# Kernel tuning notes

Measured on AMD Instinct MI355X. Metric: run time of the kernel, lower is better.

Reference implementation:

```python
import jax, jax.numpy as jnp
import numpy as np

B, S, K, N, G = 4, 2048, 4096, 11008, 128


def setup_inputs() -> dict:
    key = jax.random.key(0)
    k1, k2, k3 = jax.random.split(key, 3)
    x = jax.random.normal(k1, (B, S, K), dtype=jnp.float32)
    # packed int4 GPTQ weights: (K/8, N) int32, 8 nibbles per int32
    qweight = jax.random.randint(k2, (K // 8, N), 0, 2147483647, dtype=jnp.int32)
    # per-group scales: (K/G, N), small positive values
    scales = jax.random.uniform(k3, (K // G, N), dtype=jnp.float32) * 0.01 + 0.001
    return {"x": x, "qweight": qweight, "scales": scales, "group_size": G}


def _dequantize(qweight, scales, group_size):
    shifts = jnp.arange(0, 32, 4, dtype=jnp.int32)          # [8]
    w = (qweight[:, None, :] >> shifts[None, :, None]) & 15  # (K/8, 8, N)
    k = w.shape[0] * 8
    w = w.reshape(k, -1)                                     # (K, N) in [0, 15]
    gidx = jnp.arange(k) // group_size                       # (K,)
    # symmetric int4 dequant with per-group, per-output-channel scale
    return (w.astype(scales.dtype) - 8.0) * scales[gidx]     # (K, N)


def reference(x, qweight, scales, group_size):
    Wf = _dequantize(qweight, scales, group_size)            # (K, N)
    return jnp.einsum('bsk,kn->bsn', x, Wf)                  # (B, S, N)
```

## Files before the change

### kernel.cpp

```cpp
#include <hip/hip_runtime.h>
#include <cstdint>
#include <cstddef>

#define M_DIM 8192
#define K_DIM 4096
#define N_DIM 11008
#define NT    (K_DIM / 64)

typedef short bf16x8 __attribute__((ext_vector_type(8)));
typedef float f32x4  __attribute__((ext_vector_type(4)));
typedef unsigned short us8 __attribute__((ext_vector_type(8)));

__device__ __forceinline__ unsigned short f2bf(float f) {
  unsigned int u = __float_as_uint(f);
  u += 0x7FFFu + ((u >> 16) & 1u);
  return (unsigned short)(u >> 16);
}

__global__ __launch_bounds__(256) void cvt_x_kernel(const float* __restrict__ x,
                                                    unsigned short* __restrict__ xb) {
  const int i = blockIdx.x * 256 + threadIdx.x;
  const float4* x4 = (const float4*)x;
  float4 a = x4[(size_t)i * 2];
  float4 b = x4[(size_t)i * 2 + 1];
  us8 o;
  o[0] = f2bf(a.x); o[1] = f2bf(a.y); o[2] = f2bf(a.z); o[3] = f2bf(a.w);
  o[4] = f2bf(b.x); o[5] = f2bf(b.y); o[6] = f2bf(b.z); o[7] = f2bf(b.w);
  *(us8*)(xb + (size_t)i * 8) = o;
}

__global__ __launch_bounds__(256) void dequant_kernel(const int* __restrict__ qw,
                                                      const float* __restrict__ sc,
                                                      unsigned short* __restrict__ wt) {
  const int n0 = blockIdx.x * 64;
  const int k0 = blockIdx.y * 64;
  const int g  = blockIdx.y >> 1;
  __shared__ unsigned short lds[64 * 64];
  const int t = threadIdx.x;
  {
    const int kk_l = t >> 5;
    const int n_l  = (t & 31) * 2;
    const int key  = (n_l >> 1) & 7;
    const int2  q2 = *(const int2*)&qw[(k0 / 8 + kk_l) * N_DIM + n0 + n_l];
    const float2 s2 = *(const float2*)&sc[g * N_DIM + n0 + n_l];
    us8 o0, o1;
#pragma unroll
    for (int j = 0; j < 8; ++j) {
      o0[j] = f2bf((float)(((q2.x >> (4 * j)) & 15) - 8) * s2.x);
      o1[j] = f2bf((float)(((q2.y >> (4 * j)) & 15) - 8) * s2.y);
    }
    const int pch = (kk_l ^ key) * 8;
    *(us8*)&lds[(n_l    ) * 64 + pch] = o0;
    *(us8*)&lds[(n_l + 1) * 64 + pch] = o1;
  }
  __syncthreads();
#pragma unroll
  for (int it = 0; it < 2; ++it) {
    const int idx = t + it * 256;
    const int n_l = idx >> 3;
    const int ch  = idx & 7;
    const int pch = (ch ^ ((n_l >> 1) & 7)) * 8;
    *(us8*)&wt[(size_t)(n0 + n_l) * K_DIM + k0 + ch * 8] = *(const us8*)&lds[n_l * 64 + pch];
  }
}

__global__ __launch_bounds__(512, 2) void gemm_kernel(const unsigned short* __restrict__ A,
                                                      const unsigned short* __restrict__ Bt,
                                                      float* __restrict__ C) {
  __shared__ unsigned short lds[8][8192];
  const int t    = threadIdx.x;
  const int wave = t >> 6;
  const int lane = t & 63;
  const int l15  = lane & 15;
  const int wr   = wave >> 2;
  const int wc   = wave & 3;

  const int bid = blockIdx.x;
  const int wg  = (bid & 7) * 172 + (bid >> 3);
  const int m0  = (wg / 43) * 256;
  const int n0  = (wg % 43) * 256;

  const int sq = (t & 3) ^ ((t >> 3) & 3);
  const unsigned short* gA = A  + (size_t)(m0 + (t >> 2)) * K_DIM + sq * 8;
  const unsigned short* gB = Bt + (size_t)(n0 + (t >> 2)) * K_DIM + sq * 8;

  const int sxo   = ((lane >> 4) ^ ((l15 >> 1) & 3)) << 3;
  const int aoffA = (wr * 128 + l15) * 32 + sxo;
  const int aoffB = (wc * 64  + l15) * 32 + sxo;

  auto stage = [&](const unsigned short* gbase, unsigned short* reg, int h, int tk) {
#pragma unroll
    for (int j = 0; j < 2; ++j) {
      __builtin_amdgcn_global_load_lds(
          (const __attribute__((address_space(1))) unsigned int*)(gbase + (size_t)j * 128 * K_DIM + tk * 64 + h * 32),
          (__attribute__((address_space(3))) unsigned int*)(reg + j * 4096 + t * 8),
          16, 0, 0);
    }
  };

  f32x4 acc[8][4] = {};

  stage(gA, &lds[0][0], 0, 0);
  stage(gB, &lds[4][0], 0, 0);
  stage(gA, &lds[1][0], 1, 0);
  stage(gB, &lds[5][0], 1, 0);
  stage(gA, &lds[2][0], 0, 1);
  stage(gB, &lds[6][0], 0, 1);
  asm volatile("s_waitcnt vmcnt(4)" ::: "memory");
  __builtin_amdgcn_s_barrier();

#pragma unroll 1
  for (int tk = 0; tk < NT; ++tk) {
    const int p = tk & 1;
    const unsigned short* Ah0 = &lds[p * 2 + 0][0];
    const unsigned short* Ah1 = &lds[p * 2 + 1][0];
    const unsigned short* Bh0 = &lds[4 + p * 2 + 0][0];
    const unsigned short* Bh1 = &lds[4 + p * 2 + 1][0];
    unsigned short* stA1 = &lds[(p ^ 1) * 2 + 1][0];
    unsigned short* stB1 = &lds[4 + (p ^ 1) * 2 + 1][0];
    unsigned short* stA2 = &lds[p * 2 + 0][0];
    unsigned short* stB2 = &lds[4 + p * 2 + 0][0];

    bf16x8 a[4], b[4], a2[4];

#pragma unroll
    for (int i = 0; i < 4; ++i) a[i] = *(const bf16x8*)&Ah0[aoffA + i * 512];
#pragma unroll
    for (int i = 0; i < 4; ++i) b[i] = *(const bf16x8*)&Bh0[aoffB + i * 512];
    if (tk + 1 < NT) stage(gA, stA1, 1, tk + 1);
    __builtin_amdgcn_s_barrier();
    __builtin_amdgcn_s_setprio(1);
#pragma unroll
    for (int mi = 0; mi < 4; ++mi)
#pragma unroll
      for (int ni = 0; ni < 4; ++ni)
        acc[mi][ni] = __builtin_amdgcn_mfma_f32_16x16x32_bf16(a[mi], b[ni], acc[mi][ni], 0, 0, 0);
    __builtin_amdgcn_s_setprio(0);
    __builtin_amdgcn_s_barrier();

#pragma unroll
    for (int i = 0; i < 4; ++i) a2[i] = *(const bf16x8*)&Ah0[aoffA + (i + 4) * 512];
    if (tk + 1 < NT) stage(gB, stB1, 1, tk + 1);
    __builtin_amdgcn_s_barrier();
    __builtin_amdgcn_s_setprio(1);
#pragma unroll
    for (int mi = 0; mi < 4; ++mi)
#pragma unroll
      for (int ni = 0; ni < 4; ++ni)
        acc[mi + 4][ni] = __builtin_amdgcn_mfma_f32_16x16x32_bf16(a2[mi], b[ni], acc[mi + 4][ni], 0, 0, 0);
    __builtin_amdgcn_s_setprio(0);
    __builtin_amdgcn_s_barrier();

#pragma unroll
    for (int i = 0; i < 4; ++i) a[i] = *(const bf16x8*)&Ah1[aoffA + i * 512];
#pragma unroll
    for (int i = 0; i < 4; ++i) b[i] = *(const bf16x8*)&Bh1[aoffB + i * 512];
    if (tk + 2 < NT) stage(gA, stA2, 0, tk + 2);
    __builtin_amdgcn_s_barrier();
    __builtin_amdgcn_s_setprio(1);
#pragma unroll
    for (int mi = 0; mi < 4; ++mi)
#pragma unroll
      for (int ni = 0; ni < 4; ++ni)
        acc[mi][ni] = __builtin_amdgcn_mfma_f32_16x16x32_bf16(a[mi], b[ni], acc[mi][ni], 0, 0, 0);
    __builtin_amdgcn_s_setprio(0);
    __builtin_amdgcn_s_barrier();

#pragma unroll
    for (int i = 0; i < 4; ++i) a2[i] = *(const bf16x8*)&Ah1[aoffA + (i + 4) * 512];
    if (tk + 2 < NT) stage(gB, stB2, 0, tk + 2);
    __builtin_amdgcn_s_barrier();
    __builtin_amdgcn_s_setprio(1);
#pragma unroll
    for (int mi = 0; mi < 4; ++mi)
#pragma unroll
      for (int ni = 0; ni < 4; ++ni)
        acc[mi + 4][ni] = __builtin_amdgcn_mfma_f32_16x16x32_bf16(a2[mi], b[ni], acc[mi + 4][ni], 0, 0, 0);
    __builtin_amdgcn_s_setprio(0);
    if (tk + 2 < NT)      { asm volatile("s_waitcnt vmcnt(4)" ::: "memory"); }
    else if (tk + 1 < NT) { asm volatile("s_waitcnt vmcnt(0)" ::: "memory"); }
    __builtin_amdgcn_s_barrier();
  }

  const int cn = n0 + wc * 64 + l15;
  const int rm = m0 + wr * 128 + (lane >> 4) * 4;
#pragma unroll
  for (int mi = 0; mi < 8; ++mi)
#pragma unroll
    for (int ni = 0; ni < 4; ++ni)
#pragma unroll
      for (int r = 0; r < 4; ++r)
        C[(size_t)(rm + mi * 16 + r) * N_DIM + cn + ni * 16] = acc[mi][ni][r];
}

extern "C" void kernel_launch(void* const* d_in, const int* in_sizes, int n_in,
                              void* d_out, int out_size, void* d_ws, size_t ws_size,
                              hipStream_t stream) {
  const float* x  = (const float*)d_in[0];
  const int*   qw = (const int*)d_in[1];
  const float* sc = (const float*)d_in[2];
  float* out = (float*)d_out;

  unsigned short* xb = (unsigned short*)d_ws;
  unsigned short* wt = (unsigned short*)((char*)d_ws + (size_t)M_DIM * K_DIM * 2);

  cvt_x_kernel<<<dim3(M_DIM * K_DIM / (8 * 256)), dim3(256), 0, stream>>>(x, xb);
  dequant_kernel<<<dim3(N_DIM / 64, K_DIM / 64), dim3(256), 0, stream>>>(qw, sc, wt);
  gemm_kernel<<<dim3((N_DIM / 256) * (M_DIM / 256)), dim3(512), 0, stream>>>(xb, wt, out);
}
```

Baseline: 1.143 ms.

## Unroll GEMM K-loop by two with templated stages and finer vmcnt waits

Restructures the GEMM main loop into a two-tile unrolled body with compile-time LDS buffer pointers and constant global offsets, removing per-iteration parity and branch arithmetic. Adds mid-tile vmcnt waits so that half-tile loads are awaited earlier and at finer granularity. It also changes the block-to-tile mapping so that M varies fastest within each group, which shifts L2 reuse patterns. The risk is that the altered wait placement or the new tile order reduces overlap or cache locality.

```diff
diff --git a/kernel.cpp b/kernel.cpp
--- a/kernel.cpp
+++ b/kernel.cpp
@@ -64,123 +64,139 @@
   }
 }
 
+__device__ __forceinline__ void gl_lds(const unsigned short* g, unsigned short* l) {
+  __builtin_amdgcn_global_load_lds(
+      (const __attribute__((address_space(1))) unsigned int*)g,
+      (__attribute__((address_space(3))) unsigned int*)l, 16, 0, 0);
+}
+
+template<int N> __device__ __forceinline__ void vwait() {
+  if constexpr (N == 8) asm volatile("s_waitcnt vmcnt(8)" ::: "memory");
+  if constexpr (N == 4) asm volatile("s_waitcnt vmcnt(4)" ::: "memory");
+  if constexpr (N == 0) asm volatile("s_waitcnt vmcnt(0)" ::: "memory");
+}
+
+__device__ __forceinline__ void mfma16(const bf16x8 (&a)[4], const bf16x8 (&b)[4],
+                                       f32x4 (&acc)[8][4], int mo) {
+#pragma unroll
+  for (int mi = 0; mi < 4; ++mi)
+#pragma unroll
+    for (int ni = 0; ni < 4; ++ni)
+      acc[mi + mo][ni] = __builtin_amdgcn_mfma_f32_16x16x32_bf16(a[mi], b[ni], acc[mi + mo][ni], 0, 0, 0);
+}
+
+template<int W2N, int W1N, bool S12, bool S34>
+__device__ __forceinline__ void tile_step(
+    const unsigned short* Ah0, const unsigned short* Ah1,
+    const unsigned short* Bh0, const unsigned short* Bh1,
+    unsigned short* stA1, unsigned short* stB1,
+    unsigned short* stA2, unsigned short* stB2,
+    const unsigned short* gA0, const unsigned short* gA1,
+    const unsigned short* gB0, const unsigned short* gB1,
+    int off1, int off2, int aoffA, int aoffB, int t8,
+    f32x4 (&acc)[8][4]) {
+  bf16x8 a[4], b[4], a2[4];
+
+#pragma unroll
+  for (int i = 0; i < 4; ++i) a[i] = *(const bf16x8*)&Ah0[aoffA + i * 512];
+#pragma unroll
+  for (int i = 0; i < 4; ++i) b[i] = *(const bf16x8*)&Bh0[aoffB + i * 512];
+  if constexpr (S12) { gl_lds(gA0 + off1, stA1 + t8); gl_lds(gA1 + off1, stA1 + 4096 + t8); }
+  __builtin_amdgcn_s_barrier();
+  __builtin_amdgcn_s_setprio(1);
+  mfma16(a, b, acc, 0);
+  __builtin_amdgcn_s_setprio(0);
+  __builtin_amdgcn_s_barrier();
+
+#pragma unroll
+  for (int i = 0; i < 4; ++i) a2[i] = *(const bf16x8*)&Ah0[aoffA + (i + 4) * 512];
+  if constexpr (S12) { gl_lds(gB0 + off1, stB1 + t8); gl_lds(gB1 + off1, stB1 + 4096 + t8); }
+  __builtin_amdgcn_s_barrier();
+  __builtin_amdgcn_s_setprio(1);
+  mfma16(a2, b, acc, 4);
+  __builtin_amdgcn_s_setprio(0);
+  vwait<W2N>();
+  __builtin_amdgcn_s_barrier();
+
+#pragma unroll
+  for (int i = 0; i < 4; ++i) a[i] = *(const bf16x8*)&Ah1[aoffA + i * 512];
+#pragma unroll
+  for (int i = 0; i < 4; ++i) b[i] = *(const bf16x8*)&Bh1[aoffB + i * 512];
+  if constexpr (S34) { gl_lds(gA0 + off2, stA2 + t8); gl_lds(gA1 + off2, stA2 + 4096 + t8); }
+  __builtin_amdgcn_s_barrier();
+  __builtin_amdgcn_s_setprio(1);
+  mfma16(a, b, acc, 0);
+  __builtin_amdgcn_s_setprio(0);
+  __builtin_amdgcn_s_barrier();
+
+#pragma unroll
+  for (int i = 0; i < 4; ++i) a2[i] = *(const bf16x8*)&Ah1[aoffA + (i + 4) * 512];
+  if constexpr (S34) { gl_lds(gB0 + off2, stB2 + t8); gl_lds(gB1 + off2, stB2 + 4096 + t8); }
+  __builtin_amdgcn_s_barrier();
+  __builtin_amdgcn_s_setprio(1);
+  mfma16(a2, b, acc, 4);
+  __builtin_amdgcn_s_setprio(0);
+  vwait<W1N>();
+  __builtin_amdgcn_s_barrier();
+}
+
 __global__ __launch_bounds__(512, 2) void gemm_kernel(const unsigned short* __restrict__ A,
                                                       const unsigned short* __restrict__ Bt,
                                                       float* __restrict__ C) {
   __shared__ unsigned short lds[8][8192];
+  unsigned short* AE0 = &lds[0][0]; unsigned short* AE1 = &lds[1][0];
+  unsigned short* AO0 = &lds[2][0]; unsigned short* AO1 = &lds[3][0];
+  unsigned short* BE0 = &lds[4][0]; unsigned short* BE1 = &lds[5][0];
+  unsigned short* BO0 = &lds[6][0]; unsigned short* BO1 = &lds[7][0];
+
   const int t    = threadIdx.x;
   const int wave = t >> 6;
   const int lane = t & 63;
   const int l15  = lane & 15;
   const int wr   = wave >> 2;
   const int wc   = wave & 3;
+  const int t8   = t * 8;
 
   const int bid = blockIdx.x;
   const int wg  = (bid & 7) * 172 + (bid >> 3);
-  const int m0  = (wg / 43) * 256;
-  const int n0  = (wg % 43) * 256;
+  const int m0  = (wg & 31) * 256;
+  const int n0  = (wg >> 5) * 256;
 
   const int sq = (t & 3) ^ ((t >> 3) & 3);
-  const unsigned short* gA = A  + (size_t)(m0 + (t >> 2)) * K_DIM + sq * 8;
-  const unsigned short* gB = Bt + (size_t)(n0 + (t >> 2)) * K_DIM + sq * 8;
+  const unsigned short* gA0 = A  + (size_t)(m0 + (t >> 2)) * K_DIM + sq * 8;
+  const unsigned short* gB0 = Bt + (size_t)(n0 + (t >> 2)) * K_DIM + sq * 8;
+  const unsigned short* gA1 = gA0 + (size_t)128 * K_DIM;
+  const unsigned short* gB1 = gB0 + (size_t)128 * K_DIM;
 
   const int sxo   = ((lane >> 4) ^ ((l15 >> 1) & 3)) << 3;
   const int aoffA = (wr * 128 + l15) * 32 + sxo;
   const int aoffB = (wc * 64  + l15) * 32 + sxo;
 
-  auto stage = [&](const unsigned short* gbase, unsigned short* reg, int h, int tk) {
-#pragma unroll
-    for (int j = 0; j < 2; ++j) {
-      __builtin_amdgcn_global_load_lds(
-          (const __attribute__((address_space(1))) unsigned int*)(gbase + (size_t)j * 128 * K_DIM + tk * 64 + h * 32),
-          (__attribute__((address_space(3))) unsigned int*)(reg + j * 4096 + t * 8),
-          16, 0, 0);
-    }
-  };
-
   f32x4 acc[8][4] = {};
 
-  stage(gA, &lds[0][0], 0, 0);
-  stage(gB, &lds[4][0], 0, 0);
-  stage(gA, &lds[1][0], 1, 0);
-  stage(gB, &lds[5][0], 1, 0);
-  stage(gA, &lds[2][0], 0, 1);
-  stage(gB, &lds[6][0], 0, 1);
-  asm volatile("s_waitcnt vmcnt(4)" ::: "memory");
-  __builtin_amdgcn_s_barrier();
-
+  gl_lds(gA0,      AE0 + t8); gl_lds(gA1,      AE0 + 4096 + t8);
+  gl_lds(gB0,      BE0 + t8); gl_lds(gB1,      BE0 + 4096 + t8);
+  gl_lds(gA0 + 32, AE1 + t8); gl_lds(gA1 + 32, AE1 + 4096 + t8);
+  gl_lds(gB0 + 32, BE1 + t8); gl_lds(gB1 + 32, BE1 + 4096 + t8);
+  gl_lds(gA0 + 64, AO0 + t8); gl_lds(gA1 + 64, AO0 + 4096 + t8);
+  gl_lds(gB0 + 64, BO0 + t8); gl_lds(gB1 + 64, BO0 + 4096 + t8);
+  vwait<8>();
+  __builtin_amdgcn_s_barrier();
+
+  const unsigned short* gAr0 = gA0; const unsigned short* gAr1 = gA1;
+  const unsigned short* gBr0 = gB0; const unsigned short* gBr1 = gB1;
 #pragma unroll 1
-  for (int tk = 0; tk < NT; ++tk) {
-    const int p = tk & 1;
-    const unsigned short* Ah0 = &lds[p * 2 + 0][0];
-    const unsigned short* Ah1 = &lds[p * 2 + 1][0];
-    const unsigned short* Bh0 = &lds[4 + p * 2 + 0][0];
-    const unsigned short* Bh1 = &lds[4 + p * 2 + 1][0];
-    unsigned short* stA1 = &lds[(p ^ 1) * 2 + 1][0];
-    unsigned short* stB1 = &lds[4 + (p ^ 1) * 2 + 1][0];
-    unsigned short* stA2 = &lds[p * 2 + 0][0];
-    unsigned short* stB2 = &lds[4 + p * 2 + 0][0];
-
-    bf16x8 a[4], b[4], a2[4];
-
-#pragma unroll
-    for (int i = 0; i < 4; ++i) a[i] = *(const bf16x8*)&Ah0[aoffA + i * 512];
-#pragma unroll
-    for (int i = 0; i < 4; ++i) b[i] = *(const bf16x8*)&Bh0[aoffB + i * 512];
-    if (tk + 1 < NT) stage(gA, stA1, 1, tk + 1);
-    __builtin_amdgcn_s_barrier();
-    __builtin_amdgcn_s_setprio(1);
-#pragma unroll
-    for (int mi = 0; mi < 4; ++mi)
-#pragma unroll
-      for (int ni = 0; ni < 4; ++ni)
-        acc[mi][ni] = __builtin_amdgcn_mfma_f32_16x16x32_bf16(a[mi], b[ni], acc[mi][ni], 0, 0, 0);
-    __builtin_amdgcn_s_setprio(0);
-    __builtin_amdgcn_s_barrier();
-
-#pragma unroll
-    for (int i = 0; i < 4; ++i) a2[i] = *(const bf16x8*)&Ah0[aoffA + (i + 4) * 512];
-    if (tk + 1 < NT) stage(gB, stB1, 1, tk + 1);
-    __builtin_amdgcn_s_barrier();
-    __builtin_amdgcn_s_setprio(1);
-#pragma unroll
-    for (int mi = 0; mi < 4; ++mi)
-#pragma unroll
-      for (int ni = 0; ni < 4; ++ni)
-        acc[mi + 4][ni] = __builtin_amdgcn_mfma_f32_16x16x32_bf16(a2[mi], b[ni], acc[mi + 4][ni], 0, 0, 0);
-    __builtin_amdgcn_s_setprio(0);
-    __builtin_amdgcn_s_barrier();
-
-#pragma unroll
-    for (int i = 0; i < 4; ++i) a[i] = *(const bf16x8*)&Ah1[aoffA + i * 512];
-#pragma unroll
-    for (int i = 0; i < 4; ++i) b[i] = *(const bf16x8*)&Bh1[aoffB + i * 512];
-    if (tk + 2 < NT) stage(gA, stA2, 0, tk + 2);
-    __builtin_amdgcn_s_barrier();
-    __builtin_amdgcn_s_setprio(1);
-#pragma unroll
-    for (int mi = 0; mi < 4; ++mi)
-#pragma unroll
-      for (int ni = 0; ni < 4; ++ni)
-        acc[mi][ni] = __builtin_amdgcn_mfma_f32_16x16x32_bf16(a[mi], b[ni], acc[mi][ni], 0, 0, 0);
-    __builtin_amdgcn_s_setprio(0);
-    __builtin_amdgcn_s_barrier();
-
-#pragma unroll
-    for (int i = 0; i < 4; ++i) a2[i] = *(const bf16x8*)&Ah1[aoffA + (i + 4) * 512];
-    if (tk + 2 < NT) stage(gB, stB2, 0, tk + 2);
-    __builtin_amdgcn_s_barrier();
-    __builtin_amdgcn_s_setprio(1);
-#pragma unroll
-    for (int mi = 0; mi < 4; ++mi)
-#pragma unroll
-      for (int ni = 0; ni < 4; ++ni)
-        acc[mi + 4][ni] = __builtin_amdgcn_mfma_f32_16x16x32_bf16(a2[mi], b[ni], acc[mi + 4][ni], 0, 0, 0);
-    __builtin_amdgcn_s_setprio(0);
-    if (tk + 2 < NT)      { asm volatile("s_waitcnt vmcnt(4)" ::: "memory"); }
-    else if (tk + 1 < NT) { asm volatile("s_waitcnt vmcnt(0)" ::: "memory"); }
-    __builtin_amdgcn_s_barrier();
+  for (int e = 0; e < NT - 2; e += 2) {
+    tile_step<8, 8, true, true>(AE0, AE1, BE0, BE1, AO1, BO1, AE0, BE0,
+                                gAr0, gAr1, gBr0, gBr1, 96, 128, aoffA, aoffB, t8, acc);
+    tile_step<8, 8, true, true>(AO0, AO1, BO0, BO1, AE1, BE1, AO0, BO0,
+                                gAr0, gAr1, gBr0, gBr1, 160, 192, aoffA, aoffB, t8, acc);
+    gAr0 += 128; gAr1 += 128; gBr0 += 128; gBr1 += 128;
   }
+  tile_step<8, 4, true, false>(AE0, AE1, BE0, BE1, AO1, BO1, AE0, BE0,
+                               gAr0, gAr1, gBr0, gBr1, 96, 128, aoffA, aoffB, t8, acc);
+  tile_step<0, -1, false, false>(AO0, AO1, BO0, BO1, AE1, BE1, AO0, BO0,
+                                 gAr0, gAr1, gBr0, gBr1, 160, 192, aoffA, aoffB, t8, acc);
 
   const int cn = n0 + wc * 64 + l15;
   const int rm = m0 + wr * 128 + (lane >> 4) * 4;
```

After: 1.192 ms. 4.3% more time.
